# Performance work log

Hardware: AMD Instinct MI355X
Metric: run time of the kernel (lower is better)

## Reference

```python
import jax, jax.numpy as jnp
import numpy as np

EMB = 1024
HEADS = 16
DEPTH = EMB // HEADS
B, S = 8, 1024


def setup_inputs() -> dict:
    key = jax.random.key(0)
    ks = jax.random.split(key, 12)
    sc = 0.02
    return {
        "q": jax.random.normal(ks[0], (B, S, EMB), jnp.float32),
        "k": jax.random.normal(ks[1], (B, S, EMB), jnp.float32),
        "v": jax.random.normal(ks[2], (B, S, EMB), jnp.float32),
        # per-head Dense weights stacked: [H, EMB, DEPTH], biases [H, DEPTH]
        "Wq": jax.random.normal(ks[3], (HEADS, EMB, DEPTH), jnp.float32) * sc,
        "bq": jnp.zeros((HEADS, DEPTH), jnp.float32),
        "Wk": jax.random.normal(ks[4], (HEADS, EMB, DEPTH), jnp.float32) * sc,
        "bk": jnp.zeros((HEADS, DEPTH), jnp.float32),
        "Wv": jax.random.normal(ks[5], (HEADS, EMB, DEPTH), jnp.float32) * sc,
        "bv": jnp.zeros((HEADS, DEPTH), jnp.float32),
        # output Dense: [EMB, EMB], bias [EMB]
        "Wo": jax.random.normal(ks[6], (EMB, EMB), jnp.float32) * sc,
        "bo": jnp.zeros((EMB,), jnp.float32),
    }


def reference(q, k, v, Wq, bq, Wk, bk, Wv, bv, Wo, bo):
    # Per-head Dense projections, batched over heads via einsum.
    # qh: [B, H, S, DEPTH]
    qh = jnp.einsum("bsd,hde->bhse", q, Wq) + bq[None, :, None, :]
    kh = jnp.einsum("bsd,hde->bhse", k, Wk) + bk[None, :, None, :]
    vh = jnp.einsum("bsd,hde->bhse", v, Wv) + bv[None, :, None, :]
    # Scaled dot-product attention per head: logits [B, H, Sq, Sk]
    scale = 1.0 / jnp.sqrt(jnp.asarray(DEPTH, jnp.float32))
    logits = jnp.einsum("bhqe,bhke->bhqk", qh, kh) * scale
    attn = jax.nn.softmax(logits, axis=-1)
    ctx = jnp.einsum("bhqk,bhke->bhqe", attn, vh)  # [B, H, S, DEPTH]
    # concat heads along last axis (head order preserved)
    ctx = jnp.transpose(ctx, (0, 2, 1, 3)).reshape(B, S, EMB)
    return ctx @ Wo + bo
```

## Files before the change

kernel.cpp:

```cpp
#include <hip/hip_runtime.h>
#include <hip/hip_bf16.h>
#include <stdint.h>

typedef __bf16 bf16;
typedef __attribute__((ext_vector_type(8))) __bf16 bf16x8;
typedef __attribute__((ext_vector_type(4))) __bf16 bf16x4;
typedef __attribute__((ext_vector_type(4))) float f32x4;

#define GLD(g, l) __builtin_amdgcn_global_load_lds( \
    (const __attribute__((address_space(1))) void*)(g), \
    (__attribute__((address_space(3))) void*)(l), 16, 0, 0)

__device__ __forceinline__ f32x4 mfma16(bf16x8 a, bf16x8 b, f32x4 c) {
  return __builtin_amdgcn_mfma_f32_16x16x32_bf16(a, b, c, 0, 0, 0);
}
__device__ __forceinline__ float fexp2(float x) {
  return __builtin_amdgcn_exp2f(x);
}
__device__ __forceinline__ bf16x8 cvt8(const float4& a, const float4& b) {
  bf16x8 p;
  p[0] = (bf16)a.x; p[1] = (bf16)a.y; p[2] = (bf16)a.z; p[3] = (bf16)a.w;
  p[4] = (bf16)b.x; p[5] = (bf16)b.y; p[6] = (bf16)b.z; p[7] = (bf16)b.w;
  return p;
}

__device__ __forceinline__ void compute128(const bf16* buf, int wr, int wc,
                                           int lr, int quad,
                                           f32x4 (&acc)[4][4]) {
  bf16x8 af[4], bfr[4];
#pragma unroll
  for (int i = 0; i < 4; i++) {
    const int ra = wr + i * 16 + lr;
    const int rb = wc + i * 16 + lr;
    af[i]  = *(const bf16x8*)(buf + ra * 32 + ((quad ^ ((ra >> 1) & 3)) * 8));
    bfr[i] = *(const bf16x8*)(buf + 4096 + rb * 32 +
                              ((quad ^ ((rb >> 1) & 3)) * 8));
  }
  __builtin_amdgcn_s_setprio(1);
#pragma unroll
  for (int im = 0; im < 4; im++)
#pragma unroll
    for (int in = 0; in < 4; in++)
      acc[im][in] = mfma16(af[im], bfr[in], acc[im][in]);
  __builtin_amdgcn_s_setprio(0);
}

#define WAIT_BAR(cnt)                                            \
  asm volatile("s_waitcnt vmcnt(" #cnt ")" ::: "memory");        \
  __builtin_amdgcn_s_barrier();                                  \
  asm volatile("" ::: "memory")

__global__ void wtransA(const float* __restrict__ Wq, const float* __restrict__ Wk,
                        const float* __restrict__ Wv, const float* __restrict__ Wo,
                        bf16* __restrict__ WT, bf16* __restrict__ WoT)
{
  __shared__ bf16 t[32][33];
  const int w = blockIdx.z;
  const int tx = threadIdx.x, ty = threadIdx.y;
  if (w < 3) {
    const float* W = (w == 0) ? Wq : (w == 1) ? Wk : Wv;
    const int h = blockIdx.x >> 1;
    const int c0 = (blockIdx.x & 1) * 32;
    const int r0 = blockIdx.y * 32;
    const float* s = W + (size_t)h * 65536;
    bf16* d = WT + (size_t)w * (1 << 20) + (size_t)h * 65536;
#pragma unroll
    for (int i = 0; i < 32; i += 8)
      t[ty + i][tx] = (bf16)s[(r0 + ty + i) * 64 + c0 + tx];
    __syncthreads();
#pragma unroll
    for (int i = 0; i < 32; i += 8)
      d[(c0 + ty + i) * 1024 + r0 + tx] = t[tx][ty + i];
  } else {
    const int c0 = blockIdx.x * 32, r0 = blockIdx.y * 32;
#pragma unroll
    for (int i = 0; i < 32; i += 8)
      t[ty + i][tx] = (bf16)Wo[(r0 + ty + i) * 1024 + c0 + tx];
    __syncthreads();
#pragma unroll
    for (int i = 0; i < 32; i += 8)
      WoT[(c0 + ty + i) * 1024 + r0 + tx] = t[tx][ty + i];
  }
}

__global__ __launch_bounds__(256) void cast2(const float* __restrict__ q,
                                             const float* __restrict__ k,
                                             bf16* __restrict__ qc,
                                             bf16* __restrict__ kc)
{
  const float* s = blockIdx.y ? k : q;
  bf16* d = blockIdx.y ? kc : qc;
  const size_t i = ((size_t)blockIdx.x * 256 + threadIdx.x) * 8;
  float4 a = *(const float4*)(s + i);
  float4 b = *(const float4*)(s + i + 4);
  *(bf16x8*)(d + i) = cvt8(a, b);
}

__global__ __launch_bounds__(256) void proj_qkv(
    const bf16* __restrict__ qc, const bf16* __restrict__ kc,
    const float* __restrict__ v, const bf16* __restrict__ WT,
    const float* __restrict__ bq, const float* __restrict__ bk,
    const float* __restrict__ bv, bf16* __restrict__ qh,
    bf16* __restrict__ kh, bf16* __restrict__ vt, float cscale)
{
  __shared__ bf16 S[24576];
  const int tid = threadIdx.x;
  const int wave = tid >> 6, lane = tid & 63;
  const int lr = lane & 15, quad = lane >> 4;
  const int n0 = blockIdx.x * 128;
  const int mt = blockIdx.y;
  const int mseg = mt * 128;
  const int seg = mseg >> 13;
  const int m0 = mseg & 8191;
  const int wr = (wave >> 1) * 64, wc = (wave & 1) * 64;

  const float* bias = (seg == 0) ? bq : (seg == 1) ? bk : bv;
  const bf16* Bt = WT + (size_t)seg * (1 << 20);

  f32x4 acc[4][4];
#pragma unroll
  for (int i = 0; i < 4; i++)
#pragma unroll
    for (int j = 0; j < 4; j++)
#pragma unroll
      for (int e = 0; e < 4; e++) acc[i][j][e] = 0.f;

  const int srow = tid >> 2;
  const int sko = ((tid & 3) ^ ((srow >> 1) & 3)) * 8;
  const bf16* bPtr = Bt + (size_t)(n0 + srow) * 1024 + sko;

  int i0 = 0, i1 = 1, i2 = 2;

  if (seg < 2) {
    const bf16* Ab = (seg == 1) ? kc : qc;
    const bf16* aPtr = Ab + (size_t)(m0 + srow) * 1024 + sko;
#pragma unroll
    for (int t = 0; t < 2; ++t) {
      bf16* nb = S + t * 8192;
      GLD(aPtr + t * 32,             nb + tid * 8);
      GLD(aPtr + 64 * 1024 + t * 32, nb + 2048 + tid * 8);
      GLD(bPtr + t * 32,             nb + 4096 + tid * 8);
      GLD(bPtr + 64 * 1024 + t * 32, nb + 6144 + tid * 8);
    }
    for (int it = 0; it < 30; ++it) {
      WAIT_BAR(4);
      const int k0 = (it + 2) * 32;
      bf16* nb = S + i2 * 8192;
      GLD(aPtr + k0,             nb + tid * 8);
      GLD(aPtr + 64 * 1024 + k0, nb + 2048 + tid * 8);
      GLD(bPtr + k0,             nb + 4096 + tid * 8);
      GLD(bPtr + 64 * 1024 + k0, nb + 6144 + tid * 8);
      compute128(S + i0 * 8192, wr, wc, lr, quad, acc);
      const int t = i0; i0 = i1; i1 = i2; i2 = t;
    }
    WAIT_BAR(4);
    compute128(S + i0 * 8192, wr, wc, lr, quad, acc);
    WAIT_BAR(0);
    compute128(S + i1 * 8192, wr, wc, lr, quad, acc);
  } else {
    const int ar = tid >> 1, acb = (tid & 1) * 2;
    const int asw = (ar >> 1) & 3;
    const float* vPtr = v + (size_t)(m0 + ar) * 1024 + acb * 8;
    float4 f[4];
#pragma unroll
    for (int j = 0; j < 4; j++) f[j] = *(const float4*)(vPtr + j * 4);
    {
      *(bf16x8*)(S + ar * 32 + ((acb ^ asw) * 8))       = cvt8(f[0], f[1]);
      *(bf16x8*)(S + ar * 32 + (((acb + 1) ^ asw) * 8)) = cvt8(f[2], f[3]);
    }
    GLD(bPtr,                  S + 4096 + tid * 8);
    GLD(bPtr + 64 * 1024,      S + 6144 + tid * 8);
    GLD(bPtr + 32,             S + 8192 + 4096 + tid * 8);
    GLD(bPtr + 64 * 1024 + 32, S + 8192 + 6144 + tid * 8);
    asm volatile("s_waitcnt vmcnt(2)" ::: "memory");
    for (int it = 0; it < 32; ++it) {
      asm volatile("s_waitcnt lgkmcnt(0)" ::: "memory");
      __builtin_amdgcn_sched_barrier(0);
      __builtin_amdgcn_s_barrier();
      asm volatile("" ::: "memory");
      const bool moreA = (it + 1 < 32);
      if (moreA) {
        const int k0 = (it + 1) * 32;
#pragma unroll
        for (int j = 0; j < 4; j++) f[j] = *(const float4*)(vPtr + k0 + j * 4);
      }
      if (it + 2 < 32) {
        const int k0 = (it + 2) * 32;
        bf16* nb = S + i2 * 8192;
        GLD(bPtr + k0,             nb + 4096 + tid * 8);
        GLD(bPtr + 64 * 1024 + k0, nb + 6144 + tid * 8);
      }
      compute128(S + i0 * 8192, wr, wc, lr, quad, acc);
      if (moreA) {
        bf16* nb = S + i1 * 8192;
        *(bf16x8*)(nb + ar * 32 + ((acb ^ asw) * 8))       = cvt8(f[0], f[1]);
        *(bf16x8*)(nb + ar * 32 + (((acb + 1) ^ asw) * 8)) = cvt8(f[2], f[3]);
      }
      const int t = i0; i0 = i1; i1 = i2; i2 = t;
    }
  }

  const int qd = quad * 4;
  float bv4[4];
#pragma unroll
  for (int in = 0; in < 4; in++) bv4[in] = bias[n0 + wc + in * 16 + lr];

  if (seg < 2) {
    bf16* C = (seg == 0) ? qh : kh;
    const float cmul = (seg == 0) ? cscale : 1.0f;
#pragma unroll
    for (int im = 0; im < 4; im++) {
      const int row = m0 + wr + im * 16 + qd;
#pragma unroll
      for (int in = 0; in < 4; in++) {
        const int col = n0 + wc + in * 16 + lr;
#pragma unroll
        for (int i = 0; i < 4; i++)
          C[(size_t)(row + i) * 1024 + col] = (bf16)((acc[im][in][i] + bv4[in]) * cmul);
      }
    }
  } else {
#pragma unroll
    for (int im = 0; im < 4; im++) {
      const int row = m0 + wr + im * 16 + qd;
      const int b = row >> 10, sin = row & 1023;
#pragma unroll
      for (int in = 0; in < 4; in++) {
        const int col = n0 + wc + in * 16 + lr;
        const int h = col >> 6, e = col & 63;
        bf16x4 pk;
#pragma unroll
        for (int i = 0; i < 4; i++) pk[i] = (bf16)(acc[im][in][i] + bv4[in]);
        *(bf16x4*)(vt + (size_t)(b * 16 + h) * 65536 + e * 1024 + sin) = pk;
      }
    }
  }
}

__global__ __launch_bounds__(256) void gemm_a16_c32(
    const bf16* __restrict__ A, const bf16* __restrict__ Bt,
    const float* __restrict__ bias, float* __restrict__ C)
{
  __shared__ bf16 S[24576];
  const int tid = threadIdx.x;
  const int wave = tid >> 6, lane = tid & 63;
  const int lr = lane & 15, quad = lane >> 4;
  const int n0 = blockIdx.x * 128;
  const int m0 = blockIdx.y * 128;
  const int wr = (wave >> 1) * 64, wc = (wave & 1) * 64;

  f32x4 acc[4][4];
#pragma unroll
  for (int i = 0; i < 4; i++)
#pragma unroll
    for (int j = 0; j < 4; j++)
#pragma unroll
      for (int e = 0; e < 4; e++) acc[i][j][e] = 0.f;

  const int srow = tid >> 2;
  const int sko = ((tid & 3) ^ ((srow >> 1) & 3)) * 8;
  const bf16* aPtr = A + (size_t)(m0 + srow) * 1024 + sko;
  const bf16* bPtr = Bt + (size_t)(n0 + srow) * 1024 + sko;

  int i0 = 0, i1 = 1, i2 = 2;
#pragma unroll
  for (int t = 0; t < 2; ++t) {
    bf16* nb = S + t * 8192;
    GLD(aPtr + t * 32,             nb + tid * 8);
    GLD(aPtr + 64 * 1024 + t * 32, nb + 2048 + tid * 8);
    GLD(bPtr + t * 32,             nb + 4096 + tid * 8);
    GLD(bPtr + 64 * 1024 + t * 32, nb + 6144 + tid * 8);
  }
  for (int it = 0; it < 30; ++it) {
    WAIT_BAR(4);
    const int k0 = (it + 2) * 32;
    bf16* nb = S + i2 * 8192;
    GLD(aPtr + k0,             nb + tid * 8);
    GLD(aPtr + 64 * 1024 + k0, nb + 2048 + tid * 8);
    GLD(bPtr + k0,             nb + 4096 + tid * 8);
    GLD(bPtr + 64 * 1024 + k0, nb + 6144 + tid * 8);
    compute128(S + i0 * 8192, wr, wc, lr, quad, acc);
    const int t = i0; i0 = i1; i1 = i2; i2 = t;
  }
  WAIT_BAR(4);
  compute128(S + i0 * 8192, wr, wc, lr, quad, acc);
  WAIT_BAR(0);
  compute128(S + i1 * 8192, wr, wc, lr, quad, acc);

  const int qd = quad * 4;
  float bv4[4];
#pragma unroll
  for (int in = 0; in < 4; in++) bv4[in] = bias[n0 + wc + in * 16 + lr];
#pragma unroll
  for (int im = 0; im < 4; im++) {
    const int row = m0 + wr + im * 16 + qd;
#pragma unroll
    for (int in = 0; in < 4; in++) {
      const int col = n0 + wc + in * 16 + lr;
#pragma unroll
      for (int i = 0; i < 4; i++)
        C[(size_t)(row + i) * 1024 + col] = acc[im][in][i] + bv4[in];
    }
  }
}

__global__ __launch_bounds__(256) void attn_k(
    const bf16* Q, const bf16* __restrict__ Kh,
    const bf16* __restrict__ Vt, bf16* O)
{
  __shared__ bf16 sK[64 * 72];
  __shared__ bf16 sV[64 * 72];
  __shared__ bf16 sP[128 * 72];
  const int q0 = blockIdx.x * 128, h = blockIdx.y, b = blockIdx.z;
  const int tid = threadIdx.x, wave = tid >> 6, lane = tid & 63;
  const int lr = lane & 15, quad = lane >> 4, kq = quad * 8;
  const int wq = wave * 32;

  const bf16* Qb = Q + (size_t)(b * 1024 + q0) * 1024 + h * 64;
  const bf16* Kb = Kh + (size_t)(b * 1024) * 1024 + h * 64;
  const bf16* Vb = Vt + (size_t)(b * 16 + h) * 65536;

  bf16x8 qf[2][2];
#pragma unroll
  for (int rg = 0; rg < 2; rg++)
#pragma unroll
    for (int ks = 0; ks < 2; ks++)
      qf[rg][ks] = *(const bf16x8*)(Qb + (wq + rg * 16 + lr) * 1024 + ks * 32 + kq);

  f32x4 o[2][4];
  float rsum[2][4];
#pragma unroll
  for (int rg = 0; rg < 2; rg++) {
#pragma unroll
    for (int et = 0; et < 4; et++)
#pragma unroll
      for (int e = 0; e < 4; e++) o[rg][et][e] = 0.f;
#pragma unroll
    for (int i = 0; i < 4; i++) rsum[rg][i] = 0.f;
  }

  const int r = tid >> 3;
  const int c = (tid & 7) * 8;

  bf16x8 k1 = *(const bf16x8*)(Kb + (size_t)r * 1024 + c);
  bf16x8 k2 = *(const bf16x8*)(Kb + (size_t)(32 + r) * 1024 + c);
  bf16x8 v1 = *(const bf16x8*)(Vb + (size_t)r * 1024 + c);
  bf16x8 v2 = *(const bf16x8*)(Vb + (size_t)(32 + r) * 1024 + c);

  for (int kv0 = 0; kv0 < 1024; kv0 += 64) {
    __syncthreads();
    *(bf16x8*)(sK + r * 72 + c) = k1;
    *(bf16x8*)(sK + (32 + r) * 72 + c) = k2;
    *(bf16x8*)(sV + r * 72 + c) = v1;
    *(bf16x8*)(sV + (32 + r) * 72 + c) = v2;
    __syncthreads();
    if (kv0 + 64 < 1024) {
      k1 = *(const bf16x8*)(Kb + (size_t)(kv0 + 64 + r) * 1024 + c);
      k2 = *(const bf16x8*)(Kb + (size_t)(kv0 + 96 + r) * 1024 + c);
      v1 = *(const bf16x8*)(Vb + (size_t)r * 1024 + kv0 + 64 + c);
      v2 = *(const bf16x8*)(Vb + (size_t)(32 + r) * 1024 + kv0 + 64 + c);
    }

    f32x4 sc[2][4];
    __builtin_amdgcn_s_setprio(1);
#pragma unroll
    for (int nt = 0; nt < 4; nt++) {
      bf16x8 kf0 = *(const bf16x8*)(sK + (nt * 16 + lr) * 72 + kq);
      bf16x8 kf1 = *(const bf16x8*)(sK + (nt * 16 + lr) * 72 + 32 + kq);
#pragma unroll
      for (int rg = 0; rg < 2; rg++) {
        f32x4 z;
#pragma unroll
        for (int e = 0; e < 4; e++) z[e] = 0.f;
        z = mfma16(qf[rg][0], kf0, z);
        z = mfma16(qf[rg][1], kf1, z);
        sc[rg][nt] = z;
      }
    }
    __builtin_amdgcn_s_setprio(0);

#pragma unroll
    for (int rg = 0; rg < 2; rg++)
#pragma unroll
      for (int i = 0; i < 4; i++) {
        float p0 = fexp2(sc[rg][0][i]);
        float p1 = fexp2(sc[rg][1][i]);
        float p2 = fexp2(sc[rg][2][i]);
        float p3 = fexp2(sc[rg][3][i]);
        rsum[rg][i] += (p0 + p1) + (p2 + p3);
        const int prow = (wq + rg * 16 + quad * 4 + i) * 72;
        sP[prow + 0 * 16 + lr] = (bf16)p0;
        sP[prow + 1 * 16 + lr] = (bf16)p1;
        sP[prow + 2 * 16 + lr] = (bf16)p2;
        sP[prow + 3 * 16 + lr] = (bf16)p3;
      }
    __syncthreads();

    __builtin_amdgcn_s_setprio(1);
#pragma unroll
    for (int et = 0; et < 4; et++) {
      bf16x8 vf0 = *(const bf16x8*)(sV + (et * 16 + lr) * 72 + kq);
      bf16x8 vf1 = *(const bf16x8*)(sV + (et * 16 + lr) * 72 + 32 + kq);
#pragma unroll
      for (int rg = 0; rg < 2; rg++) {
        bf16x8 pa = *(const bf16x8*)(sP + (wq + rg * 16 + lr) * 72 + kq);
        bf16x8 pb = *(const bf16x8*)(sP + (wq + rg * 16 + lr) * 72 + 32 + kq);
        o[rg][et] = mfma16(pa, vf0, o[rg][et]);
        o[rg][et] = mfma16(pb, vf1, o[rg][et]);
      }
    }
    __builtin_amdgcn_s_setprio(0);
  }

#pragma unroll
  for (int rg = 0; rg < 2; rg++)
#pragma unroll
    for (int i = 0; i < 4; i++) {
      float rs = rsum[rg][i];
#pragma unroll
      for (int off = 1; off < 16; off <<= 1)
        rs += __shfl_xor(rs, off, 64);
      rsum[rg][i] = 1.f / rs;
    }

  bf16* Ob = O + (size_t)(b * 1024 + q0) * 1024 + h * 64;
#pragma unroll
  for (int rg = 0; rg < 2; rg++)
#pragma unroll
    for (int i = 0; i < 4; i++) {
      const int row = wq + rg * 16 + quad * 4 + i;
#pragma unroll
      for (int et = 0; et < 4; et++)
        Ob[row * 1024 + et * 16 + lr] = (bf16)(o[rg][et][i] * rsum[rg][i]);
    }
}

extern "C" void kernel_launch(void* const* d_in, const int* in_sizes, int n_in,
                              void* d_out, int out_size, void* d_ws, size_t ws_size,
                              hipStream_t stream)
{
  const float* q  = (const float*)d_in[0];
  const float* k  = (const float*)d_in[1];
  const float* v  = (const float*)d_in[2];
  const float* Wq = (const float*)d_in[3];
  const float* bq = (const float*)d_in[4];
  const float* Wk = (const float*)d_in[5];
  const float* bk = (const float*)d_in[6];
  const float* Wv = (const float*)d_in[7];
  const float* bv = (const float*)d_in[8];
  const float* Wo = (const float*)d_in[9];
  const float* bo = (const float*)d_in[10];
  float* out = (float*)d_out;
  bf16* ws = (bf16*)d_ws;

  const int MB = 1 << 20;
  bf16* WT  = ws;
  bf16* qh  = ws + 3 * MB;
  bf16* kh  = ws + 11 * MB;
  bf16* vt  = ws + 19 * MB;
  bf16* WoT = ws + 27 * MB;
  bf16* qc  = (bf16*)d_out;
  bf16* kc  = (bf16*)d_out + 8 * MB;

  const float cscale = 0.1803368801111601f;

  dim3 tb(32, 8);
  wtransA<<<dim3(32, 32, 4), tb, 0, stream>>>(Wq, Wk, Wv, Wo, WT, WoT);
  cast2<<<dim3(4096, 2), 256, 0, stream>>>(q, k, qc, kc);

  proj_qkv<<<dim3(8, 192), 256, 0, stream>>>(qc, kc, v, WT, bq, bk, bv,
                                             qh, kh, vt, cscale);

  attn_k<<<dim3(8, 16, 8), 256, 0, stream>>>(qh, kh, vt, qh);

  gemm_a16_c32<<<dim3(8, 64), 256, 0, stream>>>(qh, WoT, bo, out);
}
```

Measured before the change: 328.3 us.

## Retile QKV projection to 256x128 blocks with 8 waves and 5-stage pipeline

```diff
diff --git a/kernel.cpp b/kernel.cpp
--- a/kernel.cpp
+++ b/kernel.cpp
@@ -23,6 +23,11 @@
   p[4] = (bf16)b.x; p[5] = (bf16)b.y; p[6] = (bf16)b.z; p[7] = (bf16)b.w;
   return p;
 }
+
+#define WAIT_BAR(cnt)                                            \
+  asm volatile("s_waitcnt vmcnt(" #cnt ")" ::: "memory");        \
+  __builtin_amdgcn_s_barrier();                                  \
+  asm volatile("" ::: "memory")
 
 __device__ __forceinline__ void compute128(const bf16* buf, int wr, int wc,
                                            int lr, int quad,
@@ -44,11 +49,6 @@
       acc[im][in] = mfma16(af[im], bfr[in], acc[im][in]);
   __builtin_amdgcn_s_setprio(0);
 }
-
-#define WAIT_BAR(cnt)                                            \
-  asm volatile("s_waitcnt vmcnt(" #cnt ")" ::: "memory");        \
-  __builtin_amdgcn_s_barrier();                                  \
-  asm volatile("" ::: "memory")
 
 __global__ void wtransA(const float* __restrict__ Wq, const float* __restrict__ Wk,
                         const float* __restrict__ Wv, const float* __restrict__ Wo,
@@ -96,67 +96,90 @@
   *(bf16x8*)(d + i) = cvt8(a, b);
 }
 
-__global__ __launch_bounds__(256) void proj_qkv(
+__global__ __launch_bounds__(512) void proj_qkv(
     const bf16* __restrict__ qc, const bf16* __restrict__ kc,
     const float* __restrict__ v, const bf16* __restrict__ WT,
     const float* __restrict__ bq, const float* __restrict__ bk,
     const float* __restrict__ bv, bf16* __restrict__ qh,
     bf16* __restrict__ kh, bf16* __restrict__ vt, float cscale)
 {
-  __shared__ bf16 S[24576];
+  __shared__ bf16 S[5 * 12288];
   const int tid = threadIdx.x;
   const int wave = tid >> 6, lane = tid & 63;
   const int lr = lane & 15, quad = lane >> 4;
-  const int n0 = blockIdx.x * 128;
-  const int mt = blockIdx.y;
-  const int mseg = mt * 128;
-  const int seg = mseg >> 13;
-  const int m0 = mseg & 8191;
-  const int wr = (wave >> 1) * 64, wc = (wave & 1) * 64;
+  const int id = blockIdx.x;
+  const int n0 = (id & 7) * 128;
+  const int mt = id >> 3;
+  const int seg = mt >> 5;
+  const int m0 = (mt & 31) * 256;
+  const int wm = wave >> 2, wn = wave & 3;
+  const int wr = wm * 128;
+  const int wc = wn * 32;
 
   const float* bias = (seg == 0) ? bq : (seg == 1) ? bk : bv;
   const bf16* Bt = WT + (size_t)seg * (1 << 20);
 
-  f32x4 acc[4][4];
-#pragma unroll
-  for (int i = 0; i < 4; i++)
-#pragma unroll
-    for (int j = 0; j < 4; j++)
+  f32x4 acc[8][2];
+#pragma unroll
+  for (int i = 0; i < 8; i++)
+#pragma unroll
+    for (int j = 0; j < 2; j++)
 #pragma unroll
       for (int e = 0; e < 4; e++) acc[i][j][e] = 0.f;
 
+  const int sko = (((tid & 3) ^ ((tid >> 3) & 3))) * 8;
   const int srow = tid >> 2;
-  const int sko = ((tid & 3) ^ ((srow >> 1) & 3)) * 8;
   const bf16* bPtr = Bt + (size_t)(n0 + srow) * 1024 + sko;
 
-  int i0 = 0, i1 = 1, i2 = 2;
+  auto pair_compute = [&](const bf16* buf) {
+    bf16x8 af[8];
+#pragma unroll
+    for (int i = 0; i < 8; i++) {
+      const int ra = wr + i * 16 + lr;
+      af[i] = *(const bf16x8*)(buf + ra * 32 + ((quad ^ ((ra >> 1) & 3)) * 8));
+    }
+    const int rb0 = wc + lr;
+    bf16x8 b0 = *(const bf16x8*)(buf + 8192 + rb0 * 32 +
+                                 ((quad ^ ((rb0 >> 1) & 3)) * 8));
+    __builtin_amdgcn_s_setprio(1);
+#pragma unroll
+    for (int i = 0; i < 8; i++) acc[i][0] = mfma16(af[i], b0, acc[i][0]);
+    __builtin_amdgcn_s_setprio(0);
+    const int rb1 = wc + 16 + lr;
+    bf16x8 b1 = *(const bf16x8*)(buf + 8192 + rb1 * 32 +
+                                 ((quad ^ ((rb1 >> 1) & 3)) * 8));
+    __builtin_amdgcn_s_setprio(1);
+#pragma unroll
+    for (int i = 0; i < 8; i++) acc[i][1] = mfma16(af[i], b1, acc[i][1]);
+    __builtin_amdgcn_s_setprio(0);
+  };
 
   if (seg < 2) {
     const bf16* Ab = (seg == 1) ? kc : qc;
-    const bf16* aPtr = Ab + (size_t)(m0 + srow) * 1024 + sko;
-#pragma unroll
-    for (int t = 0; t < 2; ++t) {
-      bf16* nb = S + t * 8192;
-      GLD(aPtr + t * 32,             nb + tid * 8);
-      GLD(aPtr + 64 * 1024 + t * 32, nb + 2048 + tid * 8);
-      GLD(bPtr + t * 32,             nb + 4096 + tid * 8);
-      GLD(bPtr + 64 * 1024 + t * 32, nb + 6144 + tid * 8);
-    }
-    for (int it = 0; it < 30; ++it) {
-      WAIT_BAR(4);
-      const int k0 = (it + 2) * 32;
-      bf16* nb = S + i2 * 8192;
-      GLD(aPtr + k0,             nb + tid * 8);
-      GLD(aPtr + 64 * 1024 + k0, nb + 2048 + tid * 8);
-      GLD(bPtr + k0,             nb + 4096 + tid * 8);
-      GLD(bPtr + 64 * 1024 + k0, nb + 6144 + tid * 8);
-      compute128(S + i0 * 8192, wr, wc, lr, quad, acc);
-      const int t = i0; i0 = i1; i1 = i2; i2 = t;
-    }
-    WAIT_BAR(4);
-    compute128(S + i0 * 8192, wr, wc, lr, quad, acc);
+    const bf16* aPtr  = Ab + (size_t)(m0 + srow) * 1024 + sko;
+    const bf16* aPtr2 = aPtr + (size_t)128 * 1024;
+#pragma unroll
+    for (int t = 0; t < 3; ++t) {
+      bf16* nb = S + t * 12288;
+      GLD(aPtr  + t * 32, nb + tid * 8);
+      GLD(aPtr2 + t * 32, nb + 4096 + tid * 8);
+      GLD(bPtr  + t * 32, nb + 8192 + tid * 8);
+    }
+    for (int h = 0; h < 30; ++h) {
+      WAIT_BAR(6);
+      if (h < 29) {
+        const int k0 = (h + 3) * 32;
+        bf16* nb = S + ((h + 3) % 5) * 12288;
+        GLD(aPtr  + k0, nb + tid * 8);
+        GLD(aPtr2 + k0, nb + 4096 + tid * 8);
+        GLD(bPtr  + k0, nb + 8192 + tid * 8);
+      }
+      pair_compute(S + (h % 5) * 12288);
+    }
+    WAIT_BAR(3);
+    pair_compute(S + (30 % 5) * 12288);
     WAIT_BAR(0);
-    compute128(S + i1 * 8192, wr, wc, lr, quad, acc);
+    pair_compute(S + (31 % 5) * 12288);
   } else {
     const int ar = tid >> 1, acb = (tid & 1) * 2;
     const int asw = (ar >> 1) & 3;
@@ -168,69 +191,65 @@
       *(bf16x8*)(S + ar * 32 + ((acb ^ asw) * 8))       = cvt8(f[0], f[1]);
       *(bf16x8*)(S + ar * 32 + (((acb + 1) ^ asw) * 8)) = cvt8(f[2], f[3]);
     }
-    GLD(bPtr,                  S + 4096 + tid * 8);
-    GLD(bPtr + 64 * 1024,      S + 6144 + tid * 8);
-    GLD(bPtr + 32,             S + 8192 + 4096 + tid * 8);
-    GLD(bPtr + 64 * 1024 + 32, S + 8192 + 6144 + tid * 8);
+    GLD(bPtr,      S + 8192 + tid * 8);
+    GLD(bPtr + 32, S + 12288 + 8192 + tid * 8);
+    GLD(bPtr + 64, S + 24576 + 8192 + tid * 8);
     asm volatile("s_waitcnt vmcnt(2)" ::: "memory");
-    for (int it = 0; it < 32; ++it) {
+    for (int h = 0; h < 32; ++h) {
       asm volatile("s_waitcnt lgkmcnt(0)" ::: "memory");
       __builtin_amdgcn_sched_barrier(0);
       __builtin_amdgcn_s_barrier();
       asm volatile("" ::: "memory");
-      const bool moreA = (it + 1 < 32);
+      const bool moreA = (h + 1 < 32);
       if (moreA) {
-        const int k0 = (it + 1) * 32;
+        const int k0 = (h + 1) * 32;
 #pragma unroll
         for (int j = 0; j < 4; j++) f[j] = *(const float4*)(vPtr + k0 + j * 4);
       }
-      if (it + 2 < 32) {
-        const int k0 = (it + 2) * 32;
-        bf16* nb = S + i2 * 8192;
-        GLD(bPtr + k0,             nb + 4096 + tid * 8);
-        GLD(bPtr + 64 * 1024 + k0, nb + 6144 + tid * 8);
-      }
-      compute128(S + i0 * 8192, wr, wc, lr, quad, acc);
+      if (h + 3 < 32) {
+        const int k0 = (h + 3) * 32;
+        GLD(bPtr + k0, S + ((h + 3) % 5) * 12288 + 8192 + tid * 8);
+      }
+      pair_compute(S + (h % 5) * 12288);
       if (moreA) {
-        bf16* nb = S + i1 * 8192;
+        bf16* nb = S + ((h + 1) % 5) * 12288;
         *(bf16x8*)(nb + ar * 32 + ((acb ^ asw) * 8))       = cvt8(f[0], f[1]);
         *(bf16x8*)(nb + ar * 32 + (((acb + 1) ^ asw) * 8)) = cvt8(f[2], f[3]);
       }
-      const int t = i0; i0 = i1; i1 = i2; i2 = t;
     }
   }
 
   const int qd = quad * 4;
-  float bv4[4];
-#pragma unroll
-  for (int in = 0; in < 4; in++) bv4[in] = bias[n0 + wc + in * 16 + lr];
+  float bv2[2];
+#pragma unroll
+  for (int in = 0; in < 2; in++) bv2[in] = bias[n0 + wc + in * 16 + lr];
 
   if (seg < 2) {
     bf16* C = (seg == 0) ? qh : kh;
     const float cmul = (seg == 0) ? cscale : 1.0f;
 #pragma unroll
-    for (int im = 0; im < 4; im++) {
+    for (int im = 0; im < 8; im++) {
       const int row = m0 + wr + im * 16 + qd;
 #pragma unroll
-      for (int in = 0; in < 4; in++) {
+      for (int in = 0; in < 2; in++) {
         const int col = n0 + wc + in * 16 + lr;
 #pragma unroll
         for (int i = 0; i < 4; i++)
-          C[(size_t)(row + i) * 1024 + col] = (bf16)((acc[im][in][i] + bv4[in]) * cmul);
+          C[(size_t)(row + i) * 1024 + col] = (bf16)((acc[im][in][i] + bv2[in]) * cmul);
       }
     }
   } else {
 #pragma unroll
-    for (int im = 0; im < 4; im++) {
+    for (int im = 0; im < 8; im++) {
       const int row = m0 + wr + im * 16 + qd;
       const int b = row >> 10, sin = row & 1023;
 #pragma unroll
-      for (int in = 0; in < 4; in++) {
+      for (int in = 0; in < 2; in++) {
         const int col = n0 + wc + in * 16 + lr;
         const int h = col >> 6, e = col & 63;
         bf16x4 pk;
 #pragma unroll
-        for (int i = 0; i < 4; i++) pk[i] = (bf16)(acc[im][in][i] + bv4[in]);
+        for (int i = 0; i < 4; i++) pk[i] = (bf16)(acc[im][in][i] + bv2[in]);
         *(bf16x4*)(vt + (size_t)(b * 16 + h) * 65536 + e * 1024 + sin) = pk;
       }
     }
@@ -468,8 +487,8 @@
   wtransA<<<dim3(32, 32, 4), tb, 0, stream>>>(Wq, Wk, Wv, Wo, WT, WoT);
   cast2<<<dim3(4096, 2), 256, 0, stream>>>(q, k, qc, kc);
 
-  proj_qkv<<<dim3(8, 192), 256, 0, stream>>>(qc, kc, v, WT, bq, bk, bv,
-                                             qh, kh, vt, cscale);
+  proj_qkv<<<dim3(768), 512, 0, stream>>>(qc, kc, v, WT, bq, bk, bv,
+                                          qh, kh, vt, cscale);
 
   attn_k<<<dim3(8, 16, 8), 256, 0, stream>>>(qh, kh, vt, qh);
 
```

Result: no change. 334.8 us (+2.0%).
